# Kernel optimization log

Hardware: AMD Instinct MI355X
Metric: run time of the kernel (lower is better)

The kernel has to match this reference:

```python
import jax, jax.numpy as jnp
import numpy as np

ALPHA = 0.2  # LeakyReLU negative slope
MASK_VAL = -9e15


def setup_inputs() -> dict:
    key = jax.random.key(0)
    k1, k2, k3 = jax.random.split(key, 3)
    bs, N, d = 16, 1024, 128
    h = jax.random.normal(k1, (bs, N, d), dtype=jnp.float32)
    # nn.Linear(in, out, bias=False).weight has shape [out, in]
    W = jax.random.normal(k2, (d, d), dtype=jnp.float32) * (1.414 / np.sqrt(d))
    # a: Linear(2*out, 1) -> weight [1, 2d] flattened to [2d], bias [1]
    a_w = jax.random.normal(k3, (2 * d,), dtype=jnp.float32) * 0.1
    a_b = jnp.zeros((1,), dtype=jnp.float32)
    return {"h": h, "W": W, "a_w": a_w, "a_b": a_b}


def reference(h, W, a_w, a_b):
    # h: [bs, N, d], W: [d, d] (torch Linear weight), a_w: [2d], a_b: [1]
    bs, N, d = h.shape
    Wh = jnp.einsum('bnd,fd->bnf', h, W)  # [bs, N, d]
    # Decompose a([Wh_i ; Wh_j]) = Wh_i . a1 + Wh_j . a2 + b  (avoids O(N^2 * 2d) concat)
    a1, a2 = a_w[:d], a_w[d:]
    s1 = Wh @ a1  # [bs, N] -- source-node contribution (row index i)
    s2 = Wh @ a2  # [bs, N] -- target-node contribution (col index j)
    e = jax.nn.leaky_relu(s1[:, :, None] + s2[:, None, :] + a_b[0], negative_slope=ALPHA)
    # adj = ones - eye: mask out the diagonal (self-edges)
    diag = jnp.eye(N, dtype=bool)
    e = jnp.where(diag[None, :, :], MASK_VAL, e)
    attention = jax.nn.softmax(e, axis=-1)  # [bs, N, N]
    h_prime = jnp.einsum('bij,bjf->bif', attention, Wh)
    return jax.nn.elu(h_prime)  # concat=True applies ELU
```

## Files before the change

kernel.cpp:

```cpp
#include <hip/hip_runtime.h>
#include <hip/hip_bf16.h>
#include <stdint.h>

#define LOG2E 1.4426950408889634f

typedef float f32x4 __attribute__((ext_vector_type(4)));
typedef short s16x8 __attribute__((ext_vector_type(8)));

__device__ __forceinline__ float bf2f(uint16_t u) {
    uint32_t x = ((uint32_t)u) << 16;
    float f;
    __builtin_memcpy(&f, &x, 4);
    return f;
}
__device__ __forceinline__ uint16_t f2bf(float f) {
    uint32_t x;
    __builtin_memcpy(&x, &f, 4);
    uint32_t r = (x + 0x7fffu + ((x >> 16) & 1u)) >> 16;
    return (uint16_t)r;
}

__global__ __launch_bounds__(256) void k0_splitW(
    const float* __restrict__ W, uint16_t* __restrict__ whi, uint16_t* __restrict__ wlo)
{
    int i = blockIdx.x * 256 + threadIdx.x;
    float x = W[i];
    uint16_t hb = f2bf(x);
    whi[i] = hb;
    wlo[i] = f2bf(x - bf2f(hb));
}

__global__ __launch_bounds__(256) void k1_gemm(
    const float* __restrict__ h, const uint16_t* __restrict__ whi_,
    const uint16_t* __restrict__ wlo_,
    const float* __restrict__ aw, const float* __restrict__ ab,
    uint16_t* __restrict__ whB, float* __restrict__ s1b, float* __restrict__ s2g,
    float* __restrict__ smaxrg)
{
    __shared__ float sred[4][16][2];
    const int tid = threadIdx.x;
    const int w = tid >> 6, lane = tid & 63;
    const int q = lane >> 4, n16 = lane & 15;
    const int R0 = blockIdx.x * 16;
    const int f0 = w * 32;

    f32x4 acc[2];
    acc[0] = 0.f; acc[1] = 0.f;

    const float* hrow = h + (size_t)(R0 + n16) * 128 + q * 8;
    const uint16_t* whbase = whi_ + (size_t)(f0 + n16) * 128 + q * 8;
    const uint16_t* wlbase = wlo_ + (size_t)(f0 + n16) * 128 + q * 8;
#pragma unroll
    for (int kc = 0; kc < 4; ++kc) {
        float4 x0 = *(const float4*)(hrow + kc * 32);
        float4 x1 = *(const float4*)(hrow + kc * 32 + 4);
        float xs[8] = {x0.x, x0.y, x0.z, x0.w, x1.x, x1.y, x1.z, x1.w};
        s16x8 ahi, alo;
#pragma unroll
        for (int t = 0; t < 8; ++t) {
            uint16_t hb = f2bf(xs[t]);
            ahi[t] = (short)hb;
            alo[t] = (short)f2bf(xs[t] - bf2f(hb));
        }
#pragma unroll
        for (int fb = 0; fb < 2; ++fb) {
            s16x8 bhi = *(const s16x8*)(whbase + fb * 16 * 128 + kc * 32);
            s16x8 blo = *(const s16x8*)(wlbase + fb * 16 * 128 + kc * 32);
            acc[fb] = __builtin_amdgcn_mfma_f32_16x16x32_bf16(ahi, bhi, acc[fb], 0, 0, 0);
            acc[fb] = __builtin_amdgcn_mfma_f32_16x16x32_bf16(alo, bhi, acc[fb], 0, 0, 0);
            acc[fb] = __builtin_amdgcn_mfma_f32_16x16x32_bf16(ahi, blo, acc[fb], 0, 0, 0);
        }
    }

    float s1p[4] = {0.f, 0.f, 0.f, 0.f}, s2p[4] = {0.f, 0.f, 0.f, 0.f};
#pragma unroll
    for (int fb = 0; fb < 2; ++fb) {
        float a1 = aw[f0 + fb * 16 + n16];
        float a2 = aw[128 + f0 + fb * 16 + n16];
#pragma unroll
        for (int reg = 0; reg < 4; ++reg) {
            s1p[reg] = fmaf(acc[fb][reg], a1, s1p[reg]);
            s2p[reg] = fmaf(acc[fb][reg], a2, s2p[reg]);
        }
    }
#pragma unroll
    for (int off = 1; off < 16; off <<= 1) {
#pragma unroll
        for (int reg = 0; reg < 4; ++reg) {
            s1p[reg] += __shfl_xor(s1p[reg], off);
            s2p[reg] += __shfl_xor(s2p[reg], off);
        }
    }
    if (n16 == 0) {
#pragma unroll
        for (int reg = 0; reg < 4; ++reg) {
            sred[w][q * 4 + reg][0] = s1p[reg];
            sred[w][q * 4 + reg][1] = s2p[reg];
        }
    }
    __syncthreads();
    if (tid < 16) {
        float s1 = sred[0][tid][0] + sred[1][tid][0] + sred[2][tid][0] + sred[3][tid][0];
        float s2 = sred[0][tid][1] + sred[1][tid][1] + sred[2][tid][1] + sred[3][tid][1];
        int R = R0 + tid;
        s1b[R] = LOG2E * (s1 + ab[0]);
        float s2s = LOG2E * s2;
        s2g[R] = s2s;
        float m = s2s;
#pragma unroll
        for (int off = 1; off < 16; off <<= 1)
            m = fmaxf(m, __shfl_xor(m, off));
        if (tid == 0) smaxrg[blockIdx.x] = m;
    }

    const int b = R0 >> 10;
    const int jt = (R0 & 1023) >> 5;
    const int rg1 = (R0 >> 4) & 1;
    uint16_t* base = whB + (size_t)b * 131072 + (size_t)jt * 512;
    const int lane8p = (rg1 * 2 + (q >> 1)) * 16 + n16;
#pragma unroll
    for (int fb = 0; fb < 2; ++fb) {
        int fblk = w * 2 + fb;
        uint32_t e0 = f2bf(acc[fb][0]), e1 = f2bf(acc[fb][1]);
        uint32_t e2 = f2bf(acc[fb][2]), e3 = f2bf(acc[fb][3]);
        uint2 val = make_uint2(e0 | (e1 << 16), e2 | (e3 << 16));
        *(uint2*)(base + fblk * 16384 + lane8p * 8 + (q & 1) * 4) = val;
    }
}

__global__ __launch_bounds__(64) void k2_attn(
    const uint16_t* __restrict__ whB, const float* __restrict__ s1b,
    const float* __restrict__ s2g, const float* __restrict__ smaxrg,
    float* __restrict__ out)
{
    const int lane = threadIdx.x;
    const int q = lane >> 4, n16 = lane & 15;
    const int idx = blockIdx.x;
    const int xcd = idx & 7, o = idx >> 3;
    const int b = xcd * 2 + (o >> 8);
    const int rem = o & 255;
    const int fq = rem >> 6, rg = rem & 63;
    const int rowbase = b * 1024 + rg * 16;
    const int jb = b * 1024;

    float M = smaxrg[b * 64 + lane];
#pragma unroll
    for (int off = 1; off < 64; off <<= 1)
        M = fmaxf(M, __shfl_xor(M, off));

    const int iRow = rowbase + n16;
    const int ji = iRow & 1023;
    const float s1v = s1b[iRow];
    const float tm = s1v + M;
    const float mi = fmaxf(tm, 0.2f * tm);
    const float Ai = s1v - mi;
    const float Bi = fmaf(0.2f, s1v, -mi);
    float l = 0.f;
    f32x4 acc[2];
    acc[0] = 0.f; acc[1] = 0.f;

    const uint16_t* wb = whB + (size_t)b * 131072 + (size_t)lane * 8;
    const float* ug = s2g + jb + q * 8;

    for (int jt = 0; jt < 32; ++jt) {
        const int J0 = jt * 32;
        float4 ua = *(const float4*)(ug + J0);
        float4 ub = *(const float4*)(ug + J0 + 4);
        float uv[8] = {ua.x, ua.y, ua.z, ua.w, ub.x, ub.y, ub.z, ub.w};
        s16x8 A;
#pragma unroll
        for (int t = 0; t < 8; ++t) {
            float arg = fmaxf(Ai + uv[t], fmaf(0.2f, uv[t], Bi));
            float p = __builtin_amdgcn_exp2f(arg);
            if (J0 + q * 8 + t == ji) p = 0.f;
            uint16_t pb = f2bf(p);
            l += bf2f(pb);
            A[t] = (short)pb;
        }
        const uint16_t* bp = wb + (size_t)jt * 512;
#pragma unroll
        for (int fb = 0; fb < 2; ++fb) {
            s16x8 B = *(const s16x8*)(bp + (size_t)(fq * 2 + fb) * 16384);
            acc[fb] = __builtin_amdgcn_mfma_f32_16x16x32_bf16(A, B, acc[fb], 0, 0, 0);
        }
    }

    l += __shfl_xor(l, 16);
    l += __shfl_xor(l, 32);
    float rl[4];
#pragma unroll
    for (int reg = 0; reg < 4; ++reg)
        rl[reg] = 1.0f / __shfl(l, q * 4 + reg);

    const int f0 = fq * 32;
#pragma unroll
    for (int fb = 0; fb < 2; ++fb) {
#pragma unroll
        for (int reg = 0; reg < 4; ++reg) {
            float v = acc[fb][reg] * rl[reg];
            float e = v > 0.f ? v : (__builtin_amdgcn_exp2f(v * LOG2E) - 1.f);
            int row = rowbase + q * 4 + reg;
            out[(size_t)row * 128 + f0 + fb * 16 + n16] = e;
        }
    }
}

extern "C" void kernel_launch(void* const* d_in, const int* in_sizes, int n_in,
                              void* d_out, int out_size, void* d_ws, size_t ws_size,
                              hipStream_t stream) {
    (void)in_sizes; (void)n_in; (void)out_size; (void)ws_size;
    const float* h  = (const float*)d_in[0];
    const float* W  = (const float*)d_in[1];
    const float* aw = (const float*)d_in[2];
    const float* ab = (const float*)d_in[3];
    float* out = (float*)d_out;

    uint16_t* whB = (uint16_t*)d_ws;
    float* s1b    = (float*)((char*)d_ws + (4u << 20));
    float* s2g    = s1b + 16384;
    float* smaxrg = s2g + 16384;
    uint16_t* whi = (uint16_t*)(smaxrg + 1024);
    uint16_t* wlo = whi + 16384;

    k0_splitW<<<64, 256, 0, stream>>>(W, whi, wlo);
    k1_gemm<<<1024, 256, 0, stream>>>(h, whi, wlo, aw, ab, whB, s1b, s2g, smaxrg);
    k2_attn<<<4096, 64, 0, stream>>>(whB, s1b, s2g, smaxrg, out);
}
```

Measured before the change: 106.4 us.

## Process two row tiles per wave, compute row sums via MFMA, fix diagonal afterwards

Each attention wave now handles 32 query rows instead of 16, so every loaded Wh B-fragment feeds twice as many MFMAs and the grid is halved. The diagonal mask is taken out of the inner loop and corrected afterwards by subtracting the self-term from the accumulators. Row sums move from scalar adds to an extra MFMA against a ones matrix. The next B tile is prefetched into registers, and bf16 packing becomes truncation instead of round-to-nearest. This cuts ALU work and memory traffic per output but adds register pressure, halves parallelism, and slightly changes rounding.

Result: faster. 99.23 us (-6.7%).

```diff
diff --git a/kernel.cpp b/kernel.cpp
--- a/kernel.cpp
+++ b/kernel.cpp
@@ -6,6 +6,7 @@
 
 typedef float f32x4 __attribute__((ext_vector_type(4)));
 typedef short s16x8 __attribute__((ext_vector_type(8)));
+typedef int   i32x4 __attribute__((ext_vector_type(4)));
 
 __device__ __forceinline__ float bf2f(uint16_t u) {
     uint32_t x = ((uint32_t)u) << 16;
@@ -136,71 +137,118 @@
     const int lane = threadIdx.x;
     const int q = lane >> 4, n16 = lane & 15;
     const int idx = blockIdx.x;
-    const int xcd = idx & 7, o = idx >> 3;
-    const int b = xcd * 2 + (o >> 8);
-    const int rem = o & 255;
-    const int fq = rem >> 6, rg = rem & 63;
-    const int rowbase = b * 1024 + rg * 16;
-    const int jb = b * 1024;
-
-    float M = smaxrg[b * 64 + lane];
+    const int xcd = idx & 7;
+    const int o = idx >> 3;
+    const int b = ((o >> 7) << 3) | xcd;
+    const int rem = o & 127;
+    const int rg = rem >> 2;
+    const int fq = rem & 3;
+    const int jb = b << 10;
+    const int iw0 = rg * 32;
+    const int f0 = fq * 32;
+
+    float M = smaxrg[(b << 6) | lane];
 #pragma unroll
     for (int off = 1; off < 64; off <<= 1)
         M = fmaxf(M, __shfl_xor(M, off));
 
-    const int iRow = rowbase + n16;
-    const int ji = iRow & 1023;
-    const float s1v = s1b[iRow];
-    const float tm = s1v + M;
-    const float mi = fmaxf(tm, 0.2f * tm);
-    const float Ai = s1v - mi;
-    const float Bi = fmaf(0.2f, s1v, -mi);
-    float l = 0.f;
-    f32x4 acc[2];
-    acc[0] = 0.f; acc[1] = 0.f;
-
-    const uint16_t* wb = whB + (size_t)b * 131072 + (size_t)lane * 8;
+    float Ai[2], Bi[2];
+#pragma unroll
+    for (int rf = 0; rf < 2; ++rf) {
+        float s1v = s1b[jb + iw0 + rf * 16 + n16];
+        float tm = s1v + M;
+        float mi = fmaxf(tm, 0.2f * tm);
+        Ai[rf] = s1v - mi;
+        Bi[rf] = fmaf(0.2f, s1v, -mi);
+    }
+
+    f32x4 acc[2][2], accl[2];
+#pragma unroll
+    for (int rf = 0; rf < 2; ++rf) {
+        acc[rf][0] = 0.f; acc[rf][1] = 0.f; accl[rf] = 0.f;
+    }
+
+    s16x8 Bones;
+#pragma unroll
+    for (int t = 0; t < 8; ++t) Bones[t] = (short)0x3F80;
+
+    const uint16_t* wb = whB + ((size_t)b << 17) + lane * 8;
     const float* ug = s2g + jb + q * 8;
+    const int fblk0 = fq * 2, fblk1 = fq * 2 + 1;
+
+    s16x8 Bc0 = *(const s16x8*)(wb + fblk0 * 16384);
+    s16x8 Bc1 = *(const s16x8*)(wb + fblk1 * 16384);
 
     for (int jt = 0; jt < 32; ++jt) {
-        const int J0 = jt * 32;
-        float4 ua = *(const float4*)(ug + J0);
-        float4 ub = *(const float4*)(ug + J0 + 4);
+        const int jn = (jt < 31) ? jt + 1 : 31;
+        const uint16_t* bpn = wb + jn * 512;
+        s16x8 Bn0 = *(const s16x8*)(bpn + fblk0 * 16384);
+        s16x8 Bn1 = *(const s16x8*)(bpn + fblk1 * 16384);
+
+        float4 ua = *(const float4*)(ug + jt * 32);
+        float4 ub = *(const float4*)(ug + jt * 32 + 4);
         float uv[8] = {ua.x, ua.y, ua.z, ua.w, ub.x, ub.y, ub.z, ub.w};
-        s16x8 A;
-#pragma unroll
-        for (int t = 0; t < 8; ++t) {
-            float arg = fmaxf(Ai + uv[t], fmaf(0.2f, uv[t], Bi));
+
+        s16x8 A[2];
+#pragma unroll
+        for (int rf = 0; rf < 2; ++rf) {
+            i32x4 pk;
+#pragma unroll
+            for (int pr = 0; pr < 4; ++pr) {
+                float p0 = __builtin_amdgcn_exp2f(
+                    fmaxf(Ai[rf] + uv[2 * pr], fmaf(0.2f, uv[2 * pr], Bi[rf])));
+                float p1 = __builtin_amdgcn_exp2f(
+                    fmaxf(Ai[rf] + uv[2 * pr + 1], fmaf(0.2f, uv[2 * pr + 1], Bi[rf])));
+                pk[pr] = (int)((__builtin_bit_cast(uint32_t, p0) >> 16) |
+                               (__builtin_bit_cast(uint32_t, p1) & 0xffff0000u));
+            }
+            A[rf] = __builtin_bit_cast(s16x8, pk);
+        }
+#pragma unroll
+        for (int rf = 0; rf < 2; ++rf) {
+            acc[rf][0] = __builtin_amdgcn_mfma_f32_16x16x32_bf16(A[rf], Bc0, acc[rf][0], 0, 0, 0);
+            acc[rf][1] = __builtin_amdgcn_mfma_f32_16x16x32_bf16(A[rf], Bc1, acc[rf][1], 0, 0, 0);
+            accl[rf]   = __builtin_amdgcn_mfma_f32_16x16x32_bf16(A[rf], Bones, accl[rf], 0, 0, 0);
+        }
+        Bc0 = Bn0; Bc1 = Bn1;
+    }
+
+#pragma unroll
+    for (int rf = 0; rf < 2; ++rf) {
+#pragma unroll
+        for (int reg = 0; reg < 4; ++reg) {
+            int iw = iw0 + rf * 16 + q * 4 + reg;
+            float s1v = s1b[jb + iw];
+            float tm = s1v + M;
+            float mi = fmaxf(tm, 0.2f * tm);
+            float u_i = s2g[jb + iw];
+            float arg = fmaxf((s1v - mi) + u_i, fmaf(0.2f, u_i, fmaf(0.2f, s1v, -mi)));
             float p = __builtin_amdgcn_exp2f(arg);
-            if (J0 + q * 8 + t == ji) p = 0.f;
-            uint16_t pb = f2bf(p);
-            l += bf2f(pb);
-            A[t] = (short)pb;
-        }
-        const uint16_t* bp = wb + (size_t)jt * 512;
-#pragma unroll
-        for (int fb = 0; fb < 2; ++fb) {
-            s16x8 B = *(const s16x8*)(bp + (size_t)(fq * 2 + fb) * 16384);
-            acc[fb] = __builtin_amdgcn_mfma_f32_16x16x32_bf16(A, B, acc[fb], 0, 0, 0);
-        }
-    }
-
-    l += __shfl_xor(l, 16);
-    l += __shfl_xor(l, 32);
-    float rl[4];
-#pragma unroll
-    for (int reg = 0; reg < 4; ++reg)
-        rl[reg] = 1.0f / __shfl(l, q * 4 + reg);
-
-    const int f0 = fq * 32;
-#pragma unroll
-    for (int fb = 0; fb < 2; ++fb) {
-#pragma unroll
-        for (int reg = 0; reg < 4; ++reg) {
-            float v = acc[fb][reg] * rl[reg];
-            float e = v > 0.f ? v : (__builtin_amdgcn_exp2f(v * LOG2E) - 1.f);
-            int row = rowbase + q * 4 + reg;
-            out[(size_t)row * 128 + f0 + fb * 16 + n16] = e;
+            float pt = __builtin_bit_cast(float, __builtin_bit_cast(uint32_t, p) & 0xffff0000u);
+            accl[rf][reg] -= pt;
+            int lane_i = ((iw >> 3) & 3) * 16 + n16;
+#pragma unroll
+            for (int fb = 0; fb < 2; ++fb) {
+                size_t a = ((size_t)b << 17) + (size_t)(fq * 2 + fb) * 16384 +
+                           (size_t)(iw >> 5) * 512 + lane_i * 8 + (iw & 7);
+                float wv = bf2f(whB[a]);
+                acc[rf][fb][reg] -= pt * wv;
+            }
+        }
+    }
+
+#pragma unroll
+    for (int rf = 0; rf < 2; ++rf) {
+#pragma unroll
+        for (int reg = 0; reg < 4; ++reg) {
+            float rl = 1.0f / accl[rf][reg];
+            int row = jb + iw0 + rf * 16 + q * 4 + reg;
+#pragma unroll
+            for (int fb = 0; fb < 2; ++fb) {
+                float v = acc[rf][fb][reg] * rl;
+                float e = v > 0.f ? v : (__builtin_amdgcn_exp2f(v * LOG2E) - 1.f);
+                out[(size_t)row * 128 + f0 + fb * 16 + n16] = e;
+            }
         }
     }
 }
@@ -224,5 +272,5 @@
 
     k0_splitW<<<64, 256, 0, stream>>>(W, whi, wlo);
     k1_gemm<<<1024, 256, 0, stream>>>(h, whi, wlo, aw, ab, whB, s1b, s2g, smaxrg);
-    k2_attn<<<4096, 64, 0, stream>>>(whB, s1b, s2g, smaxrg, out);
-}
+    k2_attn<<<2048, 64, 0, stream>>>(whB, s1b, s2g, smaxrg, out);
+}
```
